# Kernel optimization log

Hardware: AMD Instinct MI355X
Metric: run time of the kernel (lower is better)

Reference implementation:

```python
import jax, jax.numpy as jnp
import numpy as np

# S4D (diagonal state space) layer, version=1, bidirectional.
# Faithful to the standard minimal S4D: ZOH-discretized diagonal kernel via
# Vandermonde, causal FFT convolution, D skip, GELU, then 1x1-conv GLU.


def _s4d(u, log_dt, C_re, C_im, log_A_real, A_imag, D_skip, W_glu, b_glu):
    # u: (B, L, H)
    B, L, Hd = u.shape
    dt = jnp.exp(log_dt)                                   # (H,)
    A = -jnp.exp(log_A_real) + 1j * A_imag                 # (H, N2) complex
    dtA = A * dt[:, None]                                  # (H, N2)
    C = (C_re + 1j * C_im) * (jnp.exp(dtA) - 1.0) / A      # (H, N2)
    V = jnp.exp(dtA[:, :, None] * jnp.arange(L))           # (H, N2, L) Vandermonde
    K = 2.0 * jnp.einsum('hn,hnl->hl', C, V).real          # (H, L) SSM kernel
    uT = jnp.swapaxes(u, 1, 2)                             # (B, H, L)
    n = 2 * L                                              # zero-pad for causal conv
    y = jnp.fft.irfft(jnp.fft.rfft(uT, n=n) * jnp.fft.rfft(K, n=n), n=n)[..., :L]
    y = y + uT * D_skip[:, None]                           # skip connection
    y = jax.nn.gelu(y, approximate=False)                  # torch nn.GELU (exact erf)
    # output_linear: Conv1d(H, 2H, 1) + GLU(dim=-2)
    z = jnp.einsum('oh,bhl->bol', W_glu, y) + b_glu[None, :, None]
    y = z[:, :Hd] * jax.nn.sigmoid(z[:, Hd:])
    return jnp.swapaxes(y, 1, 2)                           # (B, L, H)


def setup_inputs() -> dict:
    key = jax.random.key(0)
    B, L, D, N = 64, 2048, 256, 64
    N2 = N // 2
    kx, kf, kr = jax.random.split(key, 3)

    def make_params(k0):
        ks = jax.random.split(k0, 6)
        log_dt = jax.random.uniform(ks[0], (D,)) * (np.log(0.1) - np.log(0.001)) + np.log(0.001)
        C_re = jax.random.normal(ks[1], (D, N2))
        C_im = jax.random.normal(ks[2], (D, N2))
        log_A_real = jnp.log(0.5 * jnp.ones((D, N2), dtype=jnp.float32))
        A_imag = np.pi * jnp.broadcast_to(jnp.arange(N2, dtype=jnp.float32), (D, N2))
        D_skip = jax.random.normal(ks[3], (D,))
        W_glu = jax.random.normal(ks[4], (2 * D, D)) / np.sqrt(D)
        b_glu = jax.random.normal(ks[5], (2 * D,)) * 0.01
        return log_dt, C_re, C_im, log_A_real, A_imag, D_skip, W_glu, b_glu

    pf = make_params(kf)
    pr = make_params(kr)
    names = ['log_dt', 'C_re', 'C_im', 'log_A_real', 'A_imag', 'D_skip', 'W_glu', 'b_glu']
    inp = {'x': jax.random.normal(kx, (B, L, D), dtype=jnp.float32)}
    for n_, v in zip(names, pf):
        inp[n_] = v
    for n_, v in zip(names, pr):
        inp[n_ + '_rev'] = v
    return inp


def reference(x, log_dt, C_re, C_im, log_A_real, A_imag, D_skip, W_glu, b_glu,
              log_dt_rev, C_re_rev, C_im_rev, log_A_real_rev, A_imag_rev,
              D_skip_rev, W_glu_rev, b_glu_rev):
    y_fwd = _s4d(x, log_dt, C_re, C_im, log_A_real, A_imag, D_skip, W_glu, b_glu)
    y_rev = _s4d(x[:, ::-1], log_dt_rev, C_re_rev, C_im_rev, log_A_real_rev,
                 A_imag_rev, D_skip_rev, W_glu_rev, b_glu_rev)
    return y_fwd + y_rev[:, ::-1]
```

## Files before the change

kernel.cpp:

```cpp
#include <hip/hip_runtime.h>
#include <hip/hip_bf16.h>
#include <math.h>

#define Bb 64
#define Ll 2048
#define Hh 256
#define N2v 32
#define NCH 4
#define CLEN (Ll / NCH)

#define WF_OFF 1024
#define BF_OFF 525312
#define GOLD_OFF 529408
#define A2_OFF 529408
#define AF_OFF 4723712
#define WT_OFF 13112320
#define XT_OFF 13243392
#define S_OFF  80352256
#define GT_OFF 214569984
#define WS_NEED 348787712ull
#define GNEW_OFF XT_OFF

typedef __hip_bfloat16 bf16;
typedef __bf16 bf16x8 __attribute__((ext_vector_type(8)));
typedef float f32x4 __attribute__((ext_vector_type(4)));
typedef _Float16 f16;
typedef _Float16 f16x2 __attribute__((ext_vector_type(2)));
typedef _Float16 f16x4 __attribute__((ext_vector_type(4)));
typedef _Float16 f16x8 __attribute__((ext_vector_type(8)));

__device__ __forceinline__ float b2f(bf16 v) { return __bfloat162float(v); }
__device__ __forceinline__ float ldf(const float* p, int i) { return p[i]; }
__device__ __forceinline__ float ldf(const bf16* p, int i) { return b2f(p[i]); }

__device__ __forceinline__ float4 ld4f(const float* p) { return *(const float4*)p; }
__device__ __forceinline__ float4 ld4f(const bf16* p) {
  ushort4 u = *(const ushort4*)p;
  float4 r;
  r.x = b2f(*(bf16*)&u.x); r.y = b2f(*(bf16*)&u.y);
  r.z = b2f(*(bf16*)&u.z); r.w = b2f(*(bf16*)&u.w);
  return r;
}

__device__ __forceinline__ void gl2lds16(const void* g, void* l) {
  __builtin_amdgcn_global_load_lds((const __attribute__((address_space(1))) void*)g,
                                   (__attribute__((address_space(3))) void*)l, 16, 0, 0);
}

__device__ __forceinline__ f32x4 mfma16(f16x8 a, f16x8 b, f32x4 c) {
  return __builtin_amdgcn_mfma_f32_16x16x32_f16(a, b, c, 0, 0, 0);
}

__device__ __forceinline__ bool input_is_bf16(const void* logA) {
  unsigned u = *(const unsigned*)logA;
  return (u >> 16) == (u & 0xffffu);
}

__global__ void s4d_prep(const void* Wf, const void* bfb, const void* Wr,
                         const void* brb, const void* logA, char* ws) {
  const bool bf = input_is_bf16(logA);
  bf16* wdst = (bf16*)(ws + WF_OFF);
  float* bdst = (float*)(ws + BF_OFF);
  const int i = blockIdx.x * 256 + threadIdx.x;
  if (i < 262144) {
    const int dstR = i >> 8, k = i & 255;
    const int ht = dstR >> 7, c = dstR & 127;
    const int mat = c >> 5, hl = c & 31;
    const int srow = mat * 256 + ht * 32 + hl;
    const void* src = (srow < 512) ? Wf : Wr;
    const int j = ((srow < 512) ? srow : srow - 512) * 256 + k;
    const float v = bf ? b2f(((const bf16*)src)[j]) : ((const float*)src)[j];
    wdst[i] = __float2bfloat16(v);
  } else if (i < 262144 + 1024) {
    const int j = i - 262144;
    const void* src = (j < 512) ? bfb : brb;
    const int k = (j < 512) ? j : j - 512;
    bdst[j] = bf ? b2f(((const bf16*)src)[k]) : ((const float*)src)[k];
  }
}

struct ScanP {
  const void* x;
  const void* prm[2][6];
  char* ws;
};

__global__ __launch_bounds__(64) void s4d_prepA(ScanP p) {
  const int d = blockIdx.x >> 8, h = blockIdx.x & 255;
  const int lane = threadIdx.x;
  __shared__ float Ksh[64];
  char* ws = p.ws;
  const bool bf = input_is_bf16(p.prm[0][3]);
#define LDP(w_, i_) (bf ? b2f(((const bf16*)p.prm[d][w_])[i_]) : ((const float*)p.prm[d][w_])[i_])
  const float dt = expf(LDP(0, h));
  const float dsk = LDP(5, h);
  float Kv = 0.f;
  const float dl = (float)lane;
  for (int n = 0; n < 32; ++n) {
    const int idx = h * 32 + n;
    const float Ar = -expf(LDP(3, idx));
    const float Ai = LDP(4, idx);
    const float th = Ai * dt, rr = Ar * dt;
    const float er = expf(rr);
    const float wr = er * cosf(th), wi = er * sinf(th);
    const float den = 1.f / (Ar * Ar + Ai * Ai);
    const float Er = wr - 1.f, Ei = wi;
    const float qr = (Er * Ar + Ei * Ai) * den, qi = (Ei * Ar - Er * Ai) * den;
    const float CR = LDP(1, idx), CI = LDP(2, idx);
    const float cre = 2.f * (CR * qr - CI * qi), cim = 2.f * (CR * qi + CI * qr);
    const float pe = expf(rr * dl), pang = th * dl;
    Kv += cre * pe * cosf(pang) - cim * pe * sinf(pang);
  }
  Ksh[lane] = Kv;
  if (lane < 32) {
    const int idx = h * 32 + lane;
    const float Ar = -expf(LDP(3, idx));
    const float Ai = LDP(4, idx);
    const float th = Ai * dt, rr = Ar * dt;
    const float e64 = expf(rr * 64.f);
    float2 wt;
    wt.x = e64 * cosf(th * 64.f);
    wt.y = e64 * sinf(th * 64.f);
    ((float2*)(ws + WT_OFF))[(d * 256 + h) * 32 + lane] = wt;
  }
  __syncthreads();
  f16* arow = (f16*)(ws + AF_OFF) + ((size_t)(d * 256 + h) * 64 + lane) * 128;
  for (int j = 0; j < 64; ++j) {
    float v = 0.f;
    if (d == 0) { if (j <= lane) v = Ksh[lane - j]; }
    else        { if (j >= lane) v = Ksh[j - lane]; }
    if (j == lane) v += dsk;
    arow[j] = (f16)v;
  }
  const float pexp = (d == 0) ? (float)(lane + 1) : (float)(64 - lane);
  for (int n = 0; n < 32; ++n) {
    const int idx = h * 32 + n;
    const float Ar = -expf(LDP(3, idx));
    const float Ai = LDP(4, idx);
    const float th = Ai * dt, rr = Ar * dt;
    const float er = expf(rr);
    const float wr = er * cosf(th), wi = er * sinf(th);
    const float den = 1.f / (Ar * Ar + Ai * Ai);
    const float Er = wr - 1.f, Ei = wi;
    const float qr = (Er * Ar + Ei * Ai) * den, qi = (Ei * Ar - Er * Ai) * den;
    const float CR = LDP(1, idx), CI = LDP(2, idx);
    const float cre = 2.f * (CR * qr - CI * qi), cim = 2.f * (CR * qi + CI * qr);
    const float pe = expf(rr * pexp), pang = th * pexp;
    const float pwr = pe * cosf(pang), pwi = pe * sinf(pang);
    arow[64 + 2 * n]     = (f16)(cre * pwr - cim * pwi);
    arow[64 + 2 * n + 1] = (f16)(-(cre * pwi + cim * pwr));
  }
  {
    const int n = lane >> 1, im = lane & 1;
    const int idx = h * 32 + n;
    const float Ar = -expf(LDP(3, idx));
    const float Ai = LDP(4, idx);
    const float th = Ai * dt, rr = Ar * dt;
    f16* a2 = (f16*)(ws + A2_OFF) + ((size_t)h * 128 + d * 64 + lane) * 64;
    for (int i = 0; i < 64; ++i) {
      const float pp = (d == 0) ? (float)(63 - i) : (float)i;
      const float e = expf(rr * pp), ang = th * pp;
      a2[i] = (f16)(im ? e * sinf(ang) : e * cosf(ang));
    }
  }
#undef LDP
}

template <typename T>
__device__ __forceinline__ void t1_body(const T* __restrict__ x, char* ws, float* tile) {
  const int b = blockIdx.x, h0 = blockIdx.y * 64;
  const int t = threadIdx.x;
  f16* xT = (f16*)(ws + XT_OFF);
  const int h4r = (t & 15) * 4;
  const int lrb = t >> 4;
  const int hw = t & 63;
  const int lo = t >> 6;
  const int lbase = blockIdx.z * 512;
  for (int l0 = lbase; l0 < lbase + 512; l0 += 64) {
    __syncthreads();
#pragma unroll
    for (int p = 0; p < 4; ++p) {
      const int l = p * 16 + lrb;
      const float4 v = ld4f(x + ((size_t)b * 2048 + l0 + l) * 256 + h0 + h4r);
      *(float4*)&tile[l * 68 + h4r] = v;
    }
    __syncthreads();
    f16x8 o0, o1;
#pragma unroll
    for (int j = 0; j < 8; ++j) o0[j] = (f16)tile[(lo * 16 + j) * 68 + hw];
#pragma unroll
    for (int j = 0; j < 8; ++j) o1[j] = (f16)tile[(lo * 16 + 8 + j) * 68 + hw];
    f16* dst = xT + ((size_t)(h0 + hw) * 64 + b) * 2048 + l0 + lo * 16;
    *(f16x8*)dst = o0;
    *(f16x8*)(dst + 8) = o1;
  }
}

__global__ __launch_bounds__(256) void s4d_t1(const void* x, const void* logA, char* ws) {
  __shared__ float tile[64 * 68];
  if (input_is_bf16(logA)) t1_body<bf16>((const bf16*)x, ws, tile);
  else                     t1_body<float>((const float*)x, ws, tile);
}

__global__ __launch_bounds__(256, 3) void s4d_krs(char* __restrict__ ws) {
  __shared__ char lds[34816];
  const int bid = blockIdx.x;
  const int h = ((bid >> 7) << 3) | (bid & 7);
  const int cb = (bid >> 3) & 15;
  const int t = threadIdx.x, lane = t & 63, wave = t >> 6;
  const int lm = lane & 15, lq = lane >> 4;
  const f16* xT = (const f16*)(ws + XT_OFF);
  const char* a2b = ws + A2_OFF + (size_t)h * 128 * 64 * 2;
  const int srow = lane >> 3;
  const int sch = (lane & 7) ^ srow;
#pragma unroll
  for (int j = 0; j < 4; ++j) {
    const int rb = wave * 4 + j;
    const int r = rb * 8 + srow;
    gl2lds16(a2b + r * 128 + sch * 16, lds + rb * 1024);
    const int col = cb * 128 + r;
    const int b_ = col >> 5, c_ = col & 31;
    gl2lds16((const char*)(xT + ((size_t)(h * 64 + b_) * 2048 + c_ * 64)) + sch * 16,
             lds + 16384 + rb * 1024);
  }
  __syncthreads();
  f32x4 acc[2][8];
#pragma unroll
  for (int i = 0; i < 2; ++i)
#pragma unroll
    for (int j = 0; j < 8; ++j) acc[i][j] = (f32x4){0.f, 0.f, 0.f, 0.f};
#pragma unroll
  for (int kb = 0; kb < 2; ++kb) {
    const int cA = kb * 4 + lq;
    f16x8 au[2], a2f[8];
#pragma unroll
    for (int i = 0; i < 2; ++i) {
      const int r = wave * 32 + i * 16 + lm;
      au[i] = *(const f16x8*)(lds + 16384 + r * 128 + ((cA ^ (r & 7)) * 16));
    }
#pragma unroll
    for (int j = 0; j < 8; ++j) {
      const int r = j * 16 + lm;
      a2f[j] = *(const f16x8*)(lds + r * 128 + ((cA ^ (r & 7)) * 16));
    }
#pragma unroll
    for (int i = 0; i < 2; ++i)
#pragma unroll
      for (int j = 0; j < 8; ++j) acc[i][j] = mfma16(au[i], a2f[j], acc[i][j]);
  }
  __syncthreads();
  f16* Cl = (f16*)lds;
#pragma unroll
  for (int i = 0; i < 2; ++i)
#pragma unroll
    for (int j = 0; j < 8; ++j)
#pragma unroll
      for (int r = 0; r < 4; ++r)
        Cl[(wave * 32 + i * 16 + lq * 4 + r) * 136 + j * 16 + lm] = (f16)acc[i][j][r];
  __syncthreads();
  const int n = t & 31, dir = (t >> 5) & 1, bl = wave;
  const float2 wt = ((const float2*)(ws + WT_OFF))[(dir * 256 + h) * 32 + n];
  f16* Sg = (f16*)(ws + S_OFF) + ((size_t)h * 2048 + cb * 128 + bl * 32) * 128 + dir * 64 + 2 * n;
  const f16* Cr = Cl + (size_t)(bl * 32) * 136 + dir * 64 + 2 * n;
  float sr = 0.f, si = 0.f;
  const int c0 = dir ? 31 : 0, cstep = dir ? -1 : 1;
  for (int it = 0; it < 32; ++it) {
    const int c = c0 + it * cstep;
    f16x2 sv; sv[0] = (f16)sr; sv[1] = (f16)si;
    *(f16x2*)(Sg + (size_t)c * 128) = sv;
    const float rr = (float)Cr[c * 136], ri = (float)Cr[c * 136 + 1];
    const float a = sr;
    sr = wt.x * a - wt.y * si + rr;
    si = wt.x * si + wt.y * a + ri;
  }
}

__global__ __launch_bounds__(256, 2) void s4d_k3(char* __restrict__ ws) {
  __shared__ char lds[57344];
  const int bid = blockIdx.x;
  const int h = ((bid >> 8) << 3) | (bid & 7);
  const int cb = (bid >> 3) & 31;
  const int t = threadIdx.x, lane = t & 63, wave = t >> 6;
  const int lm = lane & 15, lq = lane >> 4;
  const f16* xT = (const f16*)(ws + XT_OFF);
  const char* afb = ws + AF_OFF + (size_t)h * 64 * 128 * 2;
  const char* arb = ws + AF_OFF + (size_t)(256 + h) * 64 * 128 * 2;
  const char* sb = ws + S_OFF;
  {
    const int sr4 = lane >> 4, c16 = lane & 15;
#pragma unroll
    for (int j = 0; j < 4; ++j) {
      const int rb = wave * 4 + j;
      const int r = rb * 4 + sr4;
      const int sc = c16 ^ (r & 7);
      gl2lds16(afb + r * 256 + sc * 16, lds + rb * 1024);
      gl2lds16(arb + r * 256 + sc * 16, lds + 16384 + rb * 1024);
    }
  }
  {
    const int sr8 = lane >> 3, c8 = lane & 7;
#pragma unroll
    for (int j = 0; j < 2; ++j) {
      const int rb = wave * 2 + j;
      const int clr = rb * 8 + sr8;
      const int col = cb * 64 + clr;
      const int b_ = col >> 5, c_ = col & 31;
      const int sc = c8 ^ (clr & 7);
      gl2lds16((const char*)(xT + ((size_t)(h * 64 + b_) * 2048 + c_ * 64)) + sc * 16,
               lds + 32768 + rb * 1024);
      const char* srow = sb + ((size_t)h * 2048 + col) * 256;
      gl2lds16(srow + sc * 16,       lds + 40960 + rb * 1024);
      gl2lds16(srow + 128 + sc * 16, lds + 49152 + rb * 1024);
    }
  }
  __syncthreads();
  const int dir = wave >> 1, chf = wave & 1;
  const char* At = lds + dir * 16384;
  f32x4 acc[4][2];
#pragma unroll
  for (int i = 0; i < 4; ++i)
#pragma unroll
    for (int j = 0; j < 2; ++j) acc[i][j] = (f32x4){0.f, 0.f, 0.f, 0.f};
#pragma unroll
  for (int kb = 0; kb < 4; ++kb) {
    f16x8 av[4], bv[2];
    const int cA = kb * 4 + lq;
#pragma unroll
    for (int i = 0; i < 4; ++i) {
      const int r = i * 16 + lm;
      av[i] = *(const f16x8*)(At + r * 256 + ((cA ^ (r & 7)) * 16));
    }
    const char* Bt = lds + 32768 + ((kb < 2) ? 0 : (dir ? 16384 : 8192));
    const int cB = (kb & 1) * 4 + lq;
#pragma unroll
    for (int j = 0; j < 2; ++j) {
      const int r = chf * 32 + j * 16 + lm;
      bv[j] = *(const f16x8*)(Bt + r * 128 + ((cB ^ (r & 7)) * 16));
    }
#pragma unroll
    for (int i = 0; i < 4; ++i)
#pragma unroll
      for (int j = 0; j < 2; ++j) acc[i][j] = mfma16(av[i], bv[j], acc[i][j]);
  }
  f16* gT = (f16*)(ws + GT_OFF);
#pragma unroll
  for (int i = 0; i < 4; ++i)
#pragma unroll
    for (int j = 0; j < 2; ++j) {
      const int col = cb * 64 + chf * 32 + j * 16 + lm;
      const int b_ = col >> 5, c_ = col & 31;
      const int i0 = i * 16 + lq * 4;
      f16x4 o;
#pragma unroll
      for (int r = 0; r < 4; ++r) {
        const float y = acc[i][j][r];
        o[r] = (f16)(0.5f * y * (1.f + erff(y * 0.70710678118654752f)));
      }
      *(f16x4*)(gT + ((size_t)((dir * 256 + h) * 64 + b_)) * 2048 + c_ * 64 + i0) = o;
    }
}

__global__ __launch_bounds__(256) void s4d_tr(char* __restrict__ ws) {
  const int bid = blockIdx.x;
  const int mt = bid & 7, hq = (bid >> 3) & 7, b = (bid >> 6) & 63, dir = bid >> 12;
  const int lane = threadIdx.x & 63, wave = threadIdx.x >> 6;
  const int hb = hq * 32 + wave * 8;
  const f16* gT = (const f16*)(ws + GT_OFF);
  bf16* gm = (bf16*)(ws + GNEW_OFF) + (size_t)dir * (Bb * Ll * Hh);
#pragma unroll
  for (int mp = 0; mp < 4; ++mp) {
    const size_t l = (size_t)mt * 256 + mp * 64 + lane;
    ushort us[8];
#pragma unroll
    for (int e = 0; e < 8; ++e) {
      const float f = (float)gT[((size_t)((dir * 256 + hb + e) * 64 + b)) * 2048 + l];
      bf16 bb = __float2bfloat16(f);
      us[e] = *(ushort*)&bb;
    }
    uint4 o;
    o.x = (unsigned)us[0] | ((unsigned)us[1] << 16);
    o.y = (unsigned)us[2] | ((unsigned)us[3] << 16);
    o.z = (unsigned)us[4] | ((unsigned)us[5] << 16);
    o.w = (unsigned)us[6] | ((unsigned)us[7] << 16);
    *(uint4*)((char*)gm + ((size_t)b * 2048 + l) * 512 + hb * 2) = o;
  }
}

template <typename T>
__device__ __forceinline__ void scan_body(
    const T* __restrict__ x, const T* ldt_p, const T* cre_p, const T* cim_p,
    const T* lar_p, const T* aim_p, const T* dsk_p, bf16* gbase, float2* S) {
  const int t = threadIdx.x;
  const int lane = t & 63;
  const int ch = t >> 6;
  const int hloc = lane & 7;
  const int ngrp = lane >> 3;
  const int b = blockIdx.x;
  const int hblk = blockIdx.y;
  const int dir = blockIdx.z;
  const int h = hblk * 8 + hloc;

  const float dt = expf(ldf(ldt_p, h));
  float wre[4], wim[4], cre[4], cim[4], sre[4], sim[4];
#pragma unroll
  for (int j = 0; j < 4; ++j) {
    const int idx = h * N2v + ngrp * 4 + j;
    const float Ar = -expf(ldf(lar_p, idx));
    const float Ai = ldf(aim_p, idx);
    const float er = expf(Ar * dt);
    const float wr = er * cosf(Ai * dt), wi = er * sinf(Ai * dt);
    wre[j] = wr; wim[j] = wi;
    const float Er = wr - 1.0f, Ei = wi;
    const float den = 1.0f / (Ar * Ar + Ai * Ai);
    const float qr = (Er * Ar + Ei * Ai) * den;
    const float qi = (Ei * Ar - Er * Ai) * den;
    const float CR = ldf(cre_p, idx);
    const float CI = ldf(cim_p, idx);
    cre[j] = 2.0f * (CR * qr - CI * qi);
    cim[j] = 2.0f * (CR * qi + CI * qr);
    sre[j] = 0.0f; sim[j] = 0.0f;
  }
  const float dsk = ldf(dsk_p, h);

  const int base = b * (Ll * Hh) + h;
  const int stride = dir ? -Hh : Hh;
  const T* x0 = x + base + (dir ? (Ll - 1) * Hh : 0);
  bf16* g0 = gbase + dir * (Bb * Ll * Hh) + base + (dir ? (Ll - 1) * Hh : 0);

  if (ch < NCH - 1) {
    const T* xp = x0 + ch * CLEN * stride;
    for (int it = 0; it < CLEN / 4; ++it) {
      const float u0 = ldf(xp, 0);
      const float u1 = ldf(xp, stride);
      const float u2 = ldf(xp, 2 * stride);
      const float u3 = ldf(xp, 3 * stride);
      xp += 4 * stride;
#pragma unroll
      for (int k = 0; k < 4; ++k) {
        const float U = (k == 0) ? u0 : (k == 1) ? u1 : (k == 2) ? u2 : u3;
#pragma unroll
        for (int j = 0; j < 4; ++j) {
          const float a = sre[j], bb = sim[j];
          sre[j] = fmaf(wre[j], a, fmaf(-wim[j], bb, U));
          sim[j] = fmaf(wre[j], bb, wim[j] * a);
        }
      }
    }
#pragma unroll
    for (int j = 0; j < 4; ++j)
      S[((ch * 8 + ngrp) * 4 + j) * 8 + hloc] = (float2){sre[j], sim[j]};
  }
  __syncthreads();

  float pr[4], pi[4];
#pragma unroll
  for (int j = 0; j < 4; ++j) { pr[j] = wre[j]; pi[j] = wim[j]; }
  for (int q = 0; q < 9; ++q) {
#pragma unroll
    for (int j = 0; j < 4; ++j) {
      const float a = pr[j], bb = pi[j];
      pr[j] = fmaf(a, a, -bb * bb);
      pi[j] = 2.0f * a * bb;
    }
  }
#pragma unroll
  for (int j = 0; j < 4; ++j) { sre[j] = 0.0f; sim[j] = 0.0f; }
  for (int cc = 0; cc < ch; ++cc) {
#pragma unroll
    for (int j = 0; j < 4; ++j) {
      const float2 sv = S[((cc * 8 + ngrp) * 4 + j) * 8 + hloc];
      const float a = sre[j], bb = sim[j];
      sre[j] = fmaf(pr[j], a, fmaf(-pi[j], bb, sv.x));
      sim[j] = fmaf(pr[j], bb, fmaf(pi[j], a, sv.y));
    }
  }

  const T* xp = x0 + ch * CLEN * stride;
  bf16* gp = g0 + ch * CLEN * stride;
  const bool q0 = (ngrp & 1) != 0;
  const bool q1 = (ngrp & 2) != 0;
  const bool q2 = (ngrp & 4) != 0;
  for (int it = 0; it < CLEN / 8; ++it) {
    float u[8], P[8];
#pragma unroll
    for (int k = 0; k < 8; ++k) u[k] = ldf(xp, k * stride);
    xp += 8 * stride;
#pragma unroll
    for (int k = 0; k < 8; ++k) {
      float pa = 0.0f, pb = 0.0f;
#pragma unroll
      for (int j = 0; j < 4; ++j) {
        const float a = sre[j], bb = sim[j];
        sre[j] = fmaf(wre[j], a, fmaf(-wim[j], bb, u[k]));
        sim[j] = fmaf(wre[j], bb, wim[j] * a);
        pa = fmaf(cre[j], sre[j], pa);
        pb = fmaf(cim[j], sim[j], pb);
      }
      P[k] = pa - pb;
    }
    const float Q0 = (q0 ? P[1] : P[0]) + __shfl_xor(q0 ? P[0] : P[1], 8);
    const float Q1 = (q0 ? P[3] : P[2]) + __shfl_xor(q0 ? P[2] : P[3], 8);
    const float Q2 = (q0 ? P[5] : P[4]) + __shfl_xor(q0 ? P[4] : P[5], 8);
    const float Q3 = (q0 ? P[7] : P[6]) + __shfl_xor(q0 ? P[6] : P[7], 8);
    const float R0 = (q1 ? Q1 : Q0) + __shfl_xor(q1 ? Q0 : Q1, 16);
    const float R1 = (q1 ? Q3 : Q2) + __shfl_xor(q1 ? Q2 : Q3, 16);
    const float Tt = (q2 ? R1 : R0) + __shfl_xor(q2 ? R0 : R1, 32);
    const float s01 = q0 ? u[1] : u[0];
    const float s23 = q0 ? u[3] : u[2];
    const float s45 = q0 ? u[5] : u[4];
    const float s67 = q0 ? u[7] : u[6];
    const float Uo = q2 ? (q1 ? s67 : s45) : (q1 ? s23 : s01);
    const float y = fmaf(dsk, Uo, Tt);
    const float ge = 0.5f * y * (1.0f + erff(y * 0.70710678118654752f));
    gp[ngrp * stride] = __float2bfloat16(ge);
    gp += 8 * stride;
  }
}

__global__ __launch_bounds__(256) void s4d_scan(ScanP p) {
  __shared__ float2 S[(NCH - 1) * 8 * 4 * 8];
  const int dir = blockIdx.z;
  bf16* g = (bf16*)(p.ws + GOLD_OFF);
  if (input_is_bf16(p.prm[0][3])) {
    scan_body<bf16>((const bf16*)p.x, (const bf16*)p.prm[dir][0],
                    (const bf16*)p.prm[dir][1], (const bf16*)p.prm[dir][2],
                    (const bf16*)p.prm[dir][3], (const bf16*)p.prm[dir][4],
                    (const bf16*)p.prm[dir][5], g, S);
  } else {
    scan_body<float>((const float*)p.x, (const float*)p.prm[dir][0],
                     (const float*)p.prm[dir][1], (const float*)p.prm[dir][2],
                     (const float*)p.prm[dir][3], (const float*)p.prm[dir][4],
                     (const float*)p.prm[dir][5], g, S);
  }
}

__global__ __launch_bounds__(256, 3) void s4d_glu_gemm(const char* __restrict__ ws,
                                                       void* __restrict__ out_v,
                                                       const void* logA,
                                                       unsigned goff) {
  __shared__ char lds[49152];
  const bool obf = input_is_bf16(logA);
  const char* gf = ws + goff;
  const char* gr = gf + (size_t)Bb * Ll * Hh * 2;
  const char* wre = ws + WF_OFF;
  const float* bias = (const float*)(ws + BF_OFF);

  const int lane = threadIdx.x & 63;
  const int wave = threadIdx.x >> 6;
  const int lm = lane & 15;
  const int lq = lane >> 4;
  const int bid = blockIdx.x;
  const int mt = ((bid >> 6) << 3) | (bid & 7);
  const int ht = (bid >> 3) & 7;
  const size_t mrow0 = (size_t)mt * 128;

  f32x4 acc[4][4];
#pragma unroll
  for (int i = 0; i < 4; ++i)
#pragma unroll
    for (int ct = 0; ct < 4; ++ct) acc[i][ct] = (f32x4){0.f, 0.f, 0.f, 0.f};

  const int srow16 = lane >> 2;
  const int chunk = (lane & 3) ^ ((srow16 & 3) ^ ((srow16 >> 2) & 3));

#define STAGE_KS(BUFI, KS2)                                                        \
  do {                                                                             \
    _Pragma("unroll")                                                              \
    for (int j_ = 0; j_ < 6; ++j_) {                                               \
      const int s_ = wave * 6 + j_;                                                \
      const int tile_ = s_ >> 3;                                                   \
      const int rb_ = s_ & 7;                                                      \
      const int row_ = rb_ * 16 + srow16;                                          \
      const char* gsrc_;                                                           \
      if (tile_ == 0)                                                              \
        gsrc_ = gf + (mrow0 + row_) * 512 + (KS2) * 64 + chunk * 16;               \
      else if (tile_ == 1)                                                         \
        gsrc_ = gr + (mrow0 + row_) * 512 + (KS2) * 64 + chunk * 16;               \
      else                                                                         \
        gsrc_ = wre + (size_t)(ht * 128 + row_) * 512 + (KS2) * 64 + chunk * 16;   \
      gl2lds16(gsrc_, lds + (BUFI) * 24576 + tile_ * 8192 + rb_ * 1024);           \
    }                                                                              \
  } while (0)

  STAGE_KS(0, 0);
#pragma unroll
  for (int ks = 0; ks < 8; ++ks) {
    const int buf = ks & 1;
    if (ks < 7) {
      STAGE_KS(buf ^ 1, ks + 1);
      asm volatile("s_waitcnt vmcnt(6)" ::: "memory");
    } else {
      asm volatile("s_waitcnt vmcnt(0)" ::: "memory");
    }
    __builtin_amdgcn_s_barrier();
    __builtin_amdgcn_sched_barrier(0);
    const char* Ab = lds + buf * 24576 + ((wave >> 1) ? 8192 : 0);
    const char* Bt = lds + buf * 24576 + 16384;
    bf16x8 af[4], bf_[4];
#pragma unroll
    for (int i = 0; i < 4; ++i) {
      const int r = (wave & 1) * 64 + i * 16 + lm;
      const int sw = (r & 3) ^ ((r >> 2) & 3);
      af[i] = *(const bf16x8*)(Ab + r * 64 + ((lq ^ sw) * 16));
    }
#pragma unroll
    for (int ct = 0; ct < 4; ++ct) {
      const int r = (wave >> 1) * 64 + ct * 16 + lm;
      const int sw = (r & 3) ^ ((r >> 2) & 3);
      bf_[ct] = *(const bf16x8*)(Bt + r * 64 + ((lq ^ sw) * 16));
    }
    __builtin_amdgcn_s_setprio(1);
#pragma unroll
    for (int i = 0; i < 4; ++i)
#pragma unroll
      for (int ct = 0; ct < 4; ++ct)
        acc[i][ct] = __builtin_amdgcn_mfma_f32_16x16x32_bf16(af[i], bf_[ct], acc[i][ct], 0, 0, 0);
    __builtin_amdgcn_s_setprio(0);
    __builtin_amdgcn_sched_barrier(0);
    __builtin_amdgcn_s_barrier();
    __builtin_amdgcn_sched_barrier(0);
  }
#undef STAGE_KS

  __syncthreads();
  float* xb = (float*)lds;
  if (wave >= 2) {
#pragma unroll
    for (int ctl = 0; ctl < 2; ++ctl) {
      const float blo = bias[512 + ht * 32 + ctl * 16 + lm];
      const float bhi = bias[768 + ht * 32 + ctl * 16 + lm];
#pragma unroll
      for (int i = 0; i < 4; ++i)
#pragma unroll
        for (int r = 0; r < 4; ++r) {
          const float z3 = acc[i][ctl][r] + blo;
          const float z4 = acc[i][ctl + 2][r] + bhi;
          xb[(((wave & 1) * 2 + ctl) * 16 + i * 4 + r) * 64 + lane] =
              z3 * (1.0f / (1.0f + expf(-z4)));
        }
    }
  }
  __syncthreads();
  if (wave < 2) {
#pragma unroll
    for (int ctl = 0; ctl < 2; ++ctl) {
      const int hout = ht * 32 + ctl * 16 + lm;
      const float blo = bias[hout];
      const float bhi = bias[256 + hout];
#pragma unroll
      for (int i = 0; i < 4; ++i)
#pragma unroll
        for (int r = 0; r < 4; ++r) {
          const float z1 = acc[i][ctl][r] + blo;
          const float z2 = acc[i][ctl + 2][r] + bhi;
          const float v = z1 * (1.0f / (1.0f + expf(-z2))) +
                          xb[(((wave & 1) * 2 + ctl) * 16 + i * 4 + r) * 64 + lane];
          const size_t m = mrow0 + (wave & 1) * 64 + i * 16 + lq * 4 + r;
          if (obf) ((bf16*)out_v)[m * Hh + hout] = __float2bfloat16(v);
          else     ((float*)out_v)[m * Hh + hout] = v;
        }
    }
  }
}

extern "C" void kernel_launch(void* const* d_in, const int* in_sizes, int n_in,
                              void* d_out, int out_size, void* d_ws, size_t ws_size,
                              hipStream_t stream) {
  ScanP p;
  p.x = d_in[0];
  for (int d = 0; d < 2; ++d)
    for (int j = 0; j < 6; ++j) p.prm[d][j] = d_in[1 + d * 8 + j];
  p.ws = (char*)d_ws;

  hipLaunchKernelGGL(s4d_prep, dim3(1028), dim3(256), 0, stream,
                     d_in[7], d_in[8], d_in[15], d_in[16], d_in[4], (char*)d_ws);

  if (ws_size >= (size_t)WS_NEED) {
    hipLaunchKernelGGL(s4d_prepA, dim3(512), dim3(64), 0, stream, p);
    hipLaunchKernelGGL(s4d_t1, dim3(64, 4, 4), dim3(256), 0, stream,
                       d_in[0], d_in[4], (char*)d_ws);
    hipLaunchKernelGGL(s4d_krs, dim3(4096), dim3(256), 0, stream, (char*)d_ws);
    hipLaunchKernelGGL(s4d_k3, dim3(8192), dim3(256), 0, stream, (char*)d_ws);
    hipLaunchKernelGGL(s4d_tr, dim3(8192), dim3(256), 0, stream, (char*)d_ws);
    hipLaunchKernelGGL(s4d_glu_gemm, dim3(8192), dim3(256), 0, stream,
                       (const char*)d_ws, d_out, d_in[4], (unsigned)GNEW_OFF);
  } else {
    hipLaunchKernelGGL(s4d_scan, dim3(Bb, Hh / 8, 2), dim3(256), 0, stream, p);
    hipLaunchKernelGGL(s4d_glu_gemm, dim3(8192), dim3(256), 0, stream,
                       (const char*)d_ws, d_out, d_in[4], (unsigned)GOLD_OFF);
  }
}
```

Measured before the change: 820.0 us.

## Switch GLU GEMM to fp16 with triple-buffered loads and LDS-tiled transpose

Measured after the change: 811.6 us. No clear change (-1.0%).

```diff
diff --git a/kernel.cpp b/kernel.cpp
--- a/kernel.cpp
+++ b/kernel.cpp
@@ -22,7 +22,6 @@
 #define GNEW_OFF XT_OFF
 
 typedef __hip_bfloat16 bf16;
-typedef __bf16 bf16x8 __attribute__((ext_vector_type(8)));
 typedef float f32x4 __attribute__((ext_vector_type(4)));
 typedef _Float16 f16;
 typedef _Float16 f16x2 __attribute__((ext_vector_type(2)));
@@ -59,7 +58,7 @@
 __global__ void s4d_prep(const void* Wf, const void* bfb, const void* Wr,
                          const void* brb, const void* logA, char* ws) {
   const bool bf = input_is_bf16(logA);
-  bf16* wdst = (bf16*)(ws + WF_OFF);
+  f16* wdst = (f16*)(ws + WF_OFF);
   float* bdst = (float*)(ws + BF_OFF);
   const int i = blockIdx.x * 256 + threadIdx.x;
   if (i < 262144) {
@@ -70,7 +69,7 @@
     const void* src = (srow < 512) ? Wf : Wr;
     const int j = ((srow < 512) ? srow : srow - 512) * 256 + k;
     const float v = bf ? b2f(((const bf16*)src)[j]) : ((const float*)src)[j];
-    wdst[i] = __float2bfloat16(v);
+    wdst[i] = (f16)v;
   } else if (i < 262144 + 1024) {
     const int j = i - 262144;
     const void* src = (j < 512) ? bfb : brb;
@@ -361,35 +360,37 @@
 }
 
 __global__ __launch_bounds__(256) void s4d_tr(char* __restrict__ ws) {
+  __shared__ f16 tile[32 * 80];
   const int bid = blockIdx.x;
-  const int mt = bid & 7, hq = (bid >> 3) & 7, b = (bid >> 6) & 63, dir = bid >> 12;
-  const int lane = threadIdx.x & 63, wave = threadIdx.x >> 6;
-  const int hb = hq * 32 + wave * 8;
+  const int hq = bid & 7, b = (bid >> 3) & 63, dir = bid >> 9;
+  const int t = threadIdx.x;
+  const int hb = hq * 32;
   const f16* gT = (const f16*)(ws + GT_OFF);
-  bf16* gm = (bf16*)(ws + GNEW_OFF) + (size_t)dir * (Bb * Ll * Hh);
-#pragma unroll
-  for (int mp = 0; mp < 4; ++mp) {
-    const size_t l = (size_t)mt * 256 + mp * 64 + lane;
+  f16* gm = (f16*)(ws + GNEW_OFF) + (size_t)dir * ((size_t)Bb * Ll * Hh);
+  const int hl = t >> 3, lg = t & 7;
+  const int lw = t >> 2, hc = t & 3;
+  const f16* grow = gT + ((size_t)((dir * 256 + hb + hl) * 64 + b)) * 2048 + lg * 8;
+  for (int l0 = 0; l0 < 2048; l0 += 64) {
+    __syncthreads();
+    *(f16x8*)&tile[hl * 80 + lg * 8] = *(const f16x8*)(grow + l0);
+    __syncthreads();
     ushort us[8];
 #pragma unroll
-    for (int e = 0; e < 8; ++e) {
-      const float f = (float)gT[((size_t)((dir * 256 + hb + e) * 64 + b)) * 2048 + l];
-      bf16 bb = __float2bfloat16(f);
-      us[e] = *(ushort*)&bb;
-    }
+    for (int e = 0; e < 8; ++e)
+      us[e] = *(const ushort*)&tile[(hc * 8 + e) * 80 + lw];
     uint4 o;
     o.x = (unsigned)us[0] | ((unsigned)us[1] << 16);
     o.y = (unsigned)us[2] | ((unsigned)us[3] << 16);
     o.z = (unsigned)us[4] | ((unsigned)us[5] << 16);
     o.w = (unsigned)us[6] | ((unsigned)us[7] << 16);
-    *(uint4*)((char*)gm + ((size_t)b * 2048 + l) * 512 + hb * 2) = o;
+    *(uint4*)((char*)gm + ((size_t)b * 2048 + l0 + lw) * 512 + (hb + hc * 8) * 2) = o;
   }
 }
 
 template <typename T>
 __device__ __forceinline__ void scan_body(
     const T* __restrict__ x, const T* ldt_p, const T* cre_p, const T* cim_p,
-    const T* lar_p, const T* aim_p, const T* dsk_p, bf16* gbase, float2* S) {
+    const T* lar_p, const T* aim_p, const T* dsk_p, f16* gbase, float2* S) {
   const int t = threadIdx.x;
   const int lane = t & 63;
   const int ch = t >> 6;
@@ -425,7 +426,7 @@
   const int base = b * (Ll * Hh) + h;
   const int stride = dir ? -Hh : Hh;
   const T* x0 = x + base + (dir ? (Ll - 1) * Hh : 0);
-  bf16* g0 = gbase + dir * (Bb * Ll * Hh) + base + (dir ? (Ll - 1) * Hh : 0);
+  f16* g0 = gbase + dir * (Bb * Ll * Hh) + base + (dir ? (Ll - 1) * Hh : 0);
 
   if (ch < NCH - 1) {
     const T* xp = x0 + ch * CLEN * stride;
@@ -476,7 +477,7 @@
   }
 
   const T* xp = x0 + ch * CLEN * stride;
-  bf16* gp = g0 + ch * CLEN * stride;
+  f16* gp = g0 + ch * CLEN * stride;
   const bool q0 = (ngrp & 1) != 0;
   const bool q1 = (ngrp & 2) != 0;
   const bool q2 = (ngrp & 4) != 0;
@@ -512,7 +513,7 @@
     const float Uo = q2 ? (q1 ? s67 : s45) : (q1 ? s23 : s01);
     const float y = fmaf(dsk, Uo, Tt);
     const float ge = 0.5f * y * (1.0f + erff(y * 0.70710678118654752f));
-    gp[ngrp * stride] = __float2bfloat16(ge);
+    gp[ngrp * stride] = (f16)ge;
     gp += 8 * stride;
   }
 }
@@ -520,7 +521,7 @@
 __global__ __launch_bounds__(256) void s4d_scan(ScanP p) {
   __shared__ float2 S[(NCH - 1) * 8 * 4 * 8];
   const int dir = blockIdx.z;
-  bf16* g = (bf16*)(p.ws + GOLD_OFF);
+  f16* g = (f16*)(p.ws + GOLD_OFF);
   if (input_is_bf16(p.prm[0][3])) {
     scan_body<bf16>((const bf16*)p.x, (const bf16*)p.prm[dir][0],
                     (const bf16*)p.prm[dir][1], (const bf16*)p.prm[dir][2],
@@ -534,11 +535,11 @@
   }
 }
 
-__global__ __launch_bounds__(256, 3) void s4d_glu_gemm(const char* __restrict__ ws,
+__global__ __launch_bounds__(256, 2) void s4d_glu_gemm(const char* __restrict__ ws,
                                                        void* __restrict__ out_v,
                                                        const void* logA,
                                                        unsigned goff) {
-  __shared__ char lds[49152];
+  __shared__ char lds[73728];
   const bool obf = input_is_bf16(logA);
   const char* gf = ws + goff;
   const char* gr = gf + (size_t)Bb * Ll * Hh * 2;
@@ -562,65 +563,67 @@
 
   const int srow16 = lane >> 2;
   const int chunk = (lane & 3) ^ ((srow16 & 3) ^ ((srow16 >> 2) & 3));
-
-#define STAGE_KS(BUFI, KS2)                                                        \
-  do {                                                                             \
-    _Pragma("unroll")                                                              \
-    for (int j_ = 0; j_ < 6; ++j_) {                                               \
-      const int s_ = wave * 6 + j_;                                                \
-      const int tile_ = s_ >> 3;                                                   \
-      const int rb_ = s_ & 7;                                                      \
-      const int row_ = rb_ * 16 + srow16;                                          \
-      const char* gsrc_;                                                           \
-      if (tile_ == 0)                                                              \
-        gsrc_ = gf + (mrow0 + row_) * 512 + (KS2) * 64 + chunk * 16;               \
-      else if (tile_ == 1)                                                         \
-        gsrc_ = gr + (mrow0 + row_) * 512 + (KS2) * 64 + chunk * 16;               \
-      else                                                                         \
-        gsrc_ = wre + (size_t)(ht * 128 + row_) * 512 + (KS2) * 64 + chunk * 16;   \
-      gl2lds16(gsrc_, lds + (BUFI) * 24576 + tile_ * 8192 + rb_ * 1024);           \
-    }                                                                              \
+  const char* gsrc[6];
+  unsigned ldst[6];
+#pragma unroll
+  for (int j = 0; j < 6; ++j) {
+    const int s_ = wave * 6 + j;
+    const int tile_ = s_ >> 3;
+    const int rb_ = s_ & 7;
+    const int row_ = rb_ * 16 + srow16;
+    const char* base;
+    if (tile_ == 0)      base = gf + (mrow0 + row_) * 512;
+    else if (tile_ == 1) base = gr + (mrow0 + row_) * 512;
+    else                 base = wre + (size_t)(ht * 128 + row_) * 512;
+    gsrc[j] = base + chunk * 16;
+    ldst[j] = tile_ * 8192 + rb_ * 1024;
+  }
+
+#define STAGE3(BUFI, KS2)                                                \
+  do {                                                                   \
+    _Pragma("unroll")                                                    \
+    for (int j_ = 0; j_ < 6; ++j_)                                       \
+      gl2lds16(gsrc[j_] + (KS2) * 64, lds + (BUFI) * 24576 + ldst[j_]);  \
   } while (0)
 
-  STAGE_KS(0, 0);
+  STAGE3(0, 0);
+  STAGE3(1, 1);
+  STAGE3(2, 2);
 #pragma unroll
   for (int ks = 0; ks < 8; ++ks) {
-    const int buf = ks & 1;
-    if (ks < 7) {
-      STAGE_KS(buf ^ 1, ks + 1);
-      asm volatile("s_waitcnt vmcnt(6)" ::: "memory");
-    } else {
-      asm volatile("s_waitcnt vmcnt(0)" ::: "memory");
-    }
+    if (ks <= 5)      asm volatile("s_waitcnt vmcnt(12)" ::: "memory");
+    else if (ks == 6) asm volatile("s_waitcnt vmcnt(6)" ::: "memory");
+    else              asm volatile("s_waitcnt vmcnt(0)" ::: "memory");
     __builtin_amdgcn_s_barrier();
     __builtin_amdgcn_sched_barrier(0);
+    const int buf = ks % 3;
     const char* Ab = lds + buf * 24576 + ((wave >> 1) ? 8192 : 0);
     const char* Bt = lds + buf * 24576 + 16384;
-    bf16x8 af[4], bf_[4];
+    f16x8 af[4], bf_[4];
 #pragma unroll
     for (int i = 0; i < 4; ++i) {
       const int r = (wave & 1) * 64 + i * 16 + lm;
       const int sw = (r & 3) ^ ((r >> 2) & 3);
-      af[i] = *(const bf16x8*)(Ab + r * 64 + ((lq ^ sw) * 16));
+      af[i] = *(const f16x8*)(Ab + r * 64 + ((lq ^ sw) * 16));
     }
 #pragma unroll
     for (int ct = 0; ct < 4; ++ct) {
       const int r = (wave >> 1) * 64 + ct * 16 + lm;
       const int sw = (r & 3) ^ ((r >> 2) & 3);
-      bf_[ct] = *(const bf16x8*)(Bt + r * 64 + ((lq ^ sw) * 16));
+      bf_[ct] = *(const f16x8*)(Bt + r * 64 + ((lq ^ sw) * 16));
     }
     __builtin_amdgcn_s_setprio(1);
 #pragma unroll
     for (int i = 0; i < 4; ++i)
 #pragma unroll
       for (int ct = 0; ct < 4; ++ct)
-        acc[i][ct] = __builtin_amdgcn_mfma_f32_16x16x32_bf16(af[i], bf_[ct], acc[i][ct], 0, 0, 0);
+        acc[i][ct] = mfma16(af[i], bf_[ct], acc[i][ct]);
     __builtin_amdgcn_s_setprio(0);
     __builtin_amdgcn_sched_barrier(0);
     __builtin_amdgcn_s_barrier();
-    __builtin_amdgcn_sched_barrier(0);
-  }
-#undef STAGE_KS
+    if (ks < 5) STAGE3(buf, ks + 3);
+  }
+#undef STAGE3
 
   __syncthreads();
   float* xb = (float*)lds;
@@ -681,7 +684,7 @@
                        d_in[0], d_in[4], (char*)d_ws);
     hipLaunchKernelGGL(s4d_krs, dim3(4096), dim3(256), 0, stream, (char*)d_ws);
     hipLaunchKernelGGL(s4d_k3, dim3(8192), dim3(256), 0, stream, (char*)d_ws);
-    hipLaunchKernelGGL(s4d_tr, dim3(8192), dim3(256), 0, stream, (char*)d_ws);
+    hipLaunchKernelGGL(s4d_tr, dim3(1024), dim3(256), 0, stream, (char*)d_ws);
     hipLaunchKernelGGL(s4d_glu_gemm, dim3(8192), dim3(256), 0, stream,
                        (const char*)d_ws, d_out, d_in[4], (unsigned)GNEW_OFF);
   } else {
```
